# Kernel tuning notes

Measured on AMD Instinct MI355X. Metric: run time of the kernel, lower is better.

Reference implementation:

```python
import jax, jax.numpy as jnp
import numpy as np

N = 50000      # nodes
E = 600000     # edges
D_IN = 128     # node_dim
D = 128        # out_channels
T = 4          # num_node_types
R = 4          # num_edge_types
L = 2          # num_layers
C = 8          # num_class
G = 512        # graphs in batch


def setup_inputs() -> dict:
    key = jax.random.key(0)
    ks = jax.random.split(key, 12)
    s = 0.05
    x = jax.random.normal(ks[0], (N, D_IN), jnp.float32)
    node_type = jax.random.randint(ks[1], (N,), 0, T)
    edge_index = jax.random.randint(ks[2], (2, E), 0, N)
    edge_type = jax.random.randint(ks[3], (E,), 0, R)
    batch = jnp.sort(jax.random.randint(ks[4], (N,), 0, G))
    # learned params
    W_het = jax.random.normal(ks[5], (T, D_IN, D), jnp.float32) * s
    b_het = jnp.zeros((T, D), jnp.float32)
    conv_W = jax.random.normal(ks[6], (L, R, D, D), jnp.float32) * s
    conv_b = jnp.zeros((L, R, D), jnp.float32)
    fuse_W = jax.random.normal(ks[7], (R * D, D), jnp.float32) * s
    fuse_b = jnp.zeros((D,), jnp.float32)
    cls_W = jax.random.normal(ks[8], (D, C), jnp.float32) * s
    cls_b = jnp.zeros((C,), jnp.float32)
    return dict(x=x, W_het=W_het, b_het=b_het, conv_W=conv_W, conv_b=conv_b,
                fuse_W=fuse_W, fuse_b=fuse_b, cls_W=cls_W, cls_b=cls_b,
                node_type=node_type, edge_index=edge_index, edge_type=edge_type,
                batch=batch)


def reference(x, W_het, b_het, conv_W, conv_b, fuse_W, fuse_b, cls_W, cls_b,
              node_type, edge_index, edge_type, batch):
    n = x.shape[0]
    # HeteroLinear: per-node-type linear. Compute all T projections then select.
    x_all = jnp.einsum('nd,tdo->tno', x, W_het)          # [T, N, D]
    h = x_all[node_type, jnp.arange(n)] + b_het[node_type]
    src, dst = edge_index[0], edge_index[1]
    for l in range(L):
        hs = h[src]                                       # [E, D] gather once per layer
        outs = []
        for r in range(R):
            # edges of relation r only (boolean mask == per-relation edge filtering)
            m = hs @ conv_W[l, r]                         # [E, D]
            m = m * (edge_type == r).astype(m.dtype)[:, None]
            agg = jax.ops.segment_sum(m, dst, num_segments=n)  # scatter-add to dst
            outs.append(agg + conv_b[l, r])
        h = jax.nn.relu(jnp.concatenate(outs, axis=1) @ fuse_W + fuse_b)
    # global mean pool over graphs
    counts = jax.ops.segment_sum(jnp.ones((n,), h.dtype), batch, num_segments=G)
    emb = jax.ops.segment_sum(h, batch, num_segments=G) / jnp.maximum(counts, 1.0)[:, None]
    logits = emb @ cls_W + cls_b
    return emb, logits
```

## Files before the change

### kernel.cpp

```cpp
#include <hip/hip_runtime.h>

#define N_NODES 50000
#define N_EDGES 600000
#define DIM     128
#define RR      4
#define LL      2
#define GG      512
#define CC      8
#define NB_SCAN ((N_NODES + 255) / 256)
#define EC      (N_EDGES / 4)
#define FB      ((EC + 255) / 256)
#define TB      ((N_NODES + 255) / 256)
#define NBH     ((N_NODES + 63) / 64)
#define CB      (1026 + 3125)

typedef short bf16x8 __attribute__((ext_vector_type(8)));
typedef float f32x4  __attribute__((ext_vector_type(4)));

__device__ __forceinline__ float bf16_to_f(unsigned short u) {
    return __uint_as_float(((unsigned int)u) << 16);
}
__device__ __forceinline__ unsigned short f_to_bf16(float f) {
    unsigned int u = __float_as_uint(f);
    u += 0x7FFFu + ((u >> 16) & 1u);
    return (unsigned short)(u >> 16);
}
__device__ __forceinline__ float loadf(const void* p, long i, int isbf) {
    if (isbf) return bf16_to_f(((const unsigned short*)p)[i]);
    return ((const float*)p)[i];
}
__device__ __forceinline__ void storef(void* p, long i, float v, int isbf) {
    if (isbf) ((unsigned short*)p)[i] = f_to_bf16(v);
    else      ((float*)p)[i] = v;
}

__global__ void cg_init(const unsigned int* __restrict__ xw, int* __restrict__ flag,
                        int* __restrict__ deg_tb) {
    __shared__ int cnt;
    int tid = threadIdx.x;
    int t = blockIdx.x * 256 + tid;
    if (t < N_NODES + 16) deg_tb[t] = 0;
    if (blockIdx.x == 0) {
        if (tid == 0) cnt = 0;
        __syncthreads();
        unsigned int w = xw[tid];
        unsigned int e = (w >> 7) & 0xFFu;
        atomicAdd(&cnt, (e >= 110u && e <= 133u) ? 1 : 0);
        __syncthreads();
        if (tid == 0) *flag = (cnt >= 128) ? 1 : 0;
    }
}

__global__ void cg_hist_canon(const int* __restrict__ edge_index, const int* __restrict__ node_type,
                              int* __restrict__ deg, int* __restrict__ tb,
                              const void* __restrict__ x,
                              const void* __restrict__ W_het, const void* __restrict__ b_het,
                              const void* __restrict__ conv_W, const void* __restrict__ fuse_W,
                              const void* __restrict__ conv_b, const void* __restrict__ fuse_b,
                              const int* __restrict__ flagp,
                              unsigned short* __restrict__ xb, unsigned short* __restrict__ Wt,
                              float* __restrict__ bhf,
                              unsigned short* __restrict__ M2t, float* __restrict__ cvec) {
    __shared__ float s[256];
    int bk = blockIdx.x;
    int tid = threadIdx.x;
    if (bk < FB) {
        __shared__ int loc[4];
        if (tid < 4) loc[tid] = 0;
        __syncthreads();
        int t = bk * 256 + tid;
        if (t < EC) {
            int d0 = edge_index[N_EDGES + t];
            int d1 = edge_index[N_EDGES + t + EC];
            int d2 = edge_index[N_EDGES + t + 2 * EC];
            int d3 = edge_index[N_EDGES + t + 3 * EC];
            atomicAdd(&deg[d0], 1);
            atomicAdd(&deg[d1], 1);
            atomicAdd(&deg[d2], 1);
            atomicAdd(&deg[d3], 1);
        }
        if (t < N_NODES) atomicAdd(&loc[node_type[t]], 1);
        __syncthreads();
        if (tid < 4 && loc[tid]) atomicAdd(&tb[tid], loc[tid]);
        return;
    }
    int b = bk - FB;
    int isbf = *flagp;
    if (b < 512) {
        int lr = b >> 6;
        int d  = (b & 63) * 2 + (tid >> 7);
        int r  = lr & 3;
        int o  = tid & 127;
        float acc = 0.0f;
        for (int k = 0; k < DIM; k++) {
            acc += loadf(conv_W, (long)(lr * DIM + d) * DIM + k, isbf)
                 * loadf(fuse_W, (long)(r * DIM + k) * DIM + o, isbf);
        }
        M2t[((long)lr * DIM + o) * DIM + d] = f_to_bf16(acc);
    } else if (b < 768) {
        int bc = b - 512;
        int l  = bc >> 7;
        int o  = bc & 127;
        float part = 0.0f;
        for (int rk = tid; rk < RR * DIM; rk += 256) {
            part += loadf(conv_b, (long)l * RR * DIM + rk, isbf)
                  * loadf(fuse_W, (long)rk * DIM + o, isbf);
        }
        s[tid] = part;
        __syncthreads();
        for (int off = 128; off > 0; off >>= 1) {
            if (tid < off) s[tid] += s[tid + off];
            __syncthreads();
        }
        if (tid == 0) cvec[bc] = s[0] + loadf(fuse_b, o, isbf);
    } else if (b < 1024) {
        int pair = (b - 768) * 2 + (tid >> 7);
        int t = pair >> 7;
        int o = pair & 127;
        int d = tid & 127;
        float v = loadf(W_het, ((long)t * DIM + d) * DIM + o, isbf);
        Wt[((long)t * DIM + o) * DIM + d] = f_to_bf16(v);
    } else if (b < 1026) {
        int idx = (b - 1024) * 256 + tid;
        if (idx < 4 * DIM) bhf[idx] = loadf(b_het, idx, isbf);
    } else {
        long i = ((long)(b - 1026) * 256 + tid) * 8;
        if (i >= (long)N_NODES * DIM) return;
        if (isbf) {
            *(uint4*)(xb + i) = *(const uint4*)((const unsigned short*)x + i);
        } else {
            const float* xf = (const float*)x + i;
            float4 f0 = *(const float4*)xf;
            float4 f1 = *(const float4*)(xf + 4);
            uint4 o;
            o.x = (unsigned int)f_to_bf16(f0.x) | ((unsigned int)f_to_bf16(f0.y) << 16);
            o.y = (unsigned int)f_to_bf16(f0.z) | ((unsigned int)f_to_bf16(f0.w) << 16);
            o.z = (unsigned int)f_to_bf16(f1.x) | ((unsigned int)f_to_bf16(f1.y) << 16);
            o.w = (unsigned int)f_to_bf16(f1.z) | ((unsigned int)f_to_bf16(f1.w) << 16);
            *(uint4*)(xb + i) = o;
        }
    }
}

__global__ void cg_scan_a(const int* __restrict__ deg, int* __restrict__ blocksum) {
    __shared__ int s[256];
    int tid = threadIdx.x;
    int i = blockIdx.x * 256 + tid;
    s[tid] = (i < N_NODES) ? deg[i] : 0;
    __syncthreads();
    for (int off = 128; off > 0; off >>= 1) {
        if (tid < off) s[tid] += s[tid + off];
        __syncthreads();
    }
    if (tid == 0) blocksum[blockIdx.x] = s[0];
}

__global__ void cg_scan_b(const int* __restrict__ blocksum, int* __restrict__ blockoff,
                          int* __restrict__ ccursor,
                          int* __restrict__ rowptr, int* __restrict__ tb) {
    __shared__ int s[256];
    int tid = threadIdx.x;
    int v = (tid < NB_SCAN) ? blocksum[tid] : 0;
    s[tid] = v;
    __syncthreads();
    for (int off = 1; off < 256; off <<= 1) {
        int a = (tid >= off) ? s[tid - off] : 0;
        __syncthreads();
        s[tid] += a;
        __syncthreads();
    }
    if (tid < NB_SCAN) {
        int e = s[tid] - v;
        blockoff[tid] = e;
        ccursor[tid]  = e;
    }
    if (tid == 255) rowptr[N_NODES] = s[255];
    if (tid == 0) {
        int run = 0;
        for (int t = 0; t < 4; t++) {
            tb[8 + t] = run;
            tb[4 + t] = run;
            run += tb[t];
        }
        tb[12] = run;
    }
}

__global__ void cg_scan_tfill(const int* __restrict__ deg, const int* __restrict__ blockoff,
                              int* __restrict__ rowptr,
                              const int* __restrict__ node_type, int* __restrict__ tb,
                              int* __restrict__ tlist) {
    int bk = blockIdx.x;
    int tid = threadIdx.x;
    if (bk < NB_SCAN) {
        __shared__ int s[256];
        int i = bk * 256 + tid;
        int v = (i < N_NODES) ? deg[i] : 0;
        s[tid] = v;
        __syncthreads();
        for (int off = 1; off < 256; off <<= 1) {
            int a = (tid >= off) ? s[tid - off] : 0;
            __syncthreads();
            s[tid] += a;
            __syncthreads();
        }
        if (i < N_NODES) rowptr[i] = blockoff[bk] + s[tid] - v;
    } else {
        __shared__ int lcur[4];
        __shared__ int lbase[4];
        if (tid < 4) lcur[tid] = 0;
        __syncthreads();
        int n = (bk - NB_SCAN) * 256 + tid;
        int slot = -1, t = 0;
        if (n < N_NODES) {
            t = node_type[n];
            slot = atomicAdd(&lcur[t], 1);
        }
        __syncthreads();
        if (tid < 4) lbase[tid] = atomicAdd(&tb[4 + tid], lcur[tid]);
        __syncthreads();
        if (n < N_NODES) tlist[lbase[t] + slot] = n;
    }
}

#define APAD 136

__global__ void cg_sortA_hetero(const int* __restrict__ edge_index, const int* __restrict__ edge_type,
                                int* __restrict__ ccursor, int2* __restrict__ tmp2,
                                const unsigned short* __restrict__ xb,
                                const unsigned short* __restrict__ Wt,
                                const float* __restrict__ bhf,
                                const int* __restrict__ tlist, const int* __restrict__ tb,
                                unsigned short* __restrict__ h) {
    __shared__ unsigned short a_lds[64][APAD];
    __shared__ unsigned short b_lds[DIM][APAD];
    int bk = blockIdx.x;
    int tx = threadIdx.x;
    if (bk < FB) {
        __shared__ int lhist[NB_SCAN];
        __shared__ int lbase[NB_SCAN];
        for (int i = tx; i < NB_SCAN; i += 256) lhist[i] = 0;
        __syncthreads();
        int t = bk * 256 + tx;
        int d[4], cb[4], ls[4], pl[4];
        bool act = (t < EC);
        if (act) {
#pragma unroll
            for (int k = 0; k < 4; k++) {
                int e = t + k * EC;
                d[k]  = edge_index[N_EDGES + e];
                pl[k] = (edge_index[e] << 2) | edge_type[e];
                cb[k] = d[k] >> 8;
                ls[k] = atomicAdd(&lhist[cb[k]], 1);
            }
        }
        __syncthreads();
        for (int i = tx; i < NB_SCAN; i += 256)
            lbase[i] = lhist[i] ? atomicAdd(&ccursor[i], lhist[i]) : 0;
        __syncthreads();
        if (act) {
#pragma unroll
            for (int k = 0; k < 4; k++) {
                int pos = lbase[cb[k]] + ls[k];
                tmp2[pos] = make_int2(pl[k], d[k]);
            }
        }
        return;
    }
    int bb = bk - FB;
    int t    = bb / NBH;
    int nblk = bb - t * NBH;
    int rows_base = tb[8 + t] + nblk * 64;
    int rend = tb[8 + t + 1];
    if (rows_base >= rend) return;
    const unsigned short* Wsrc = Wt + (long)t * DIM * DIM;
    for (int i = tx; i < 2048; i += 256) {
        uint4 w = *(const uint4*)(Wsrc + i * 8);
        int o = i >> 4, d2 = (i & 15) * 8;
        *(uint4*)&b_lds[o][d2] = w;
    }
    for (int i = tx; i < 1024; i += 256) {
        int row = i >> 4, seg = (i & 15) * 8;
        int gr = rows_base + row;
        uint4 w = make_uint4(0u, 0u, 0u, 0u);
        if (gr < rend) {
            int n = tlist[gr];
            w = *(const uint4*)(xb + (long)n * DIM + seg);
        }
        *(uint4*)&a_lds[row][seg] = w;
    }
    __syncthreads();
    int wv = tx >> 6, lane = tx & 63;
    int m16 = lane & 15, quad = lane >> 4;
    f32x4 acc[8];
#pragma unroll
    for (int c = 0; c < 8; c++) acc[c] = (f32x4){0.f, 0.f, 0.f, 0.f};
    for (int ks = 0; ks < 4; ks++) {
        int koff = ks * 32 + quad * 8;
        bf16x8 af = *(const bf16x8*)(const void*)&a_lds[wv * 16 + m16][koff];
#pragma unroll
        for (int c = 0; c < 8; c++) {
            bf16x8 bfr = *(const bf16x8*)(const void*)&b_lds[c * 16 + m16][koff];
            acc[c] = __builtin_amdgcn_mfma_f32_16x16x32_bf16(af, bfr, acc[c], 0, 0, 0);
        }
    }
    __syncthreads();
#pragma unroll
    for (int c = 0; c < 8; c++) {
#pragma unroll
        for (int i = 0; i < 4; i++) {
            int row = wv * 16 + quad * 4 + i;
            int col = c * 16 + m16;
            a_lds[row][col] = f_to_bf16(acc[c][i] + bhf[t * DIM + col]);
        }
    }
    __syncthreads();
    for (int i = tx; i < 1024; i += 256) {
        int row = i >> 4, seg = (i & 15) * 8;
        int gr = rows_base + row;
        if (gr < rend) {
            int n = tlist[gr];
            *(uint4*)(h + (long)n * DIM + seg) = *(const uint4*)&a_lds[row][seg];
        }
    }
}

__global__ void cg_sortB_pgemm(const int2* __restrict__ tmp2, const int* __restrict__ blockoff,
                               const int* __restrict__ rowptr, int* __restrict__ eidx,
                               const unsigned short* __restrict__ h,
                               const unsigned short* __restrict__ M2t,
                               unsigned short* __restrict__ P) {
    __shared__ unsigned short a_lds[64][APAD];
    __shared__ unsigned short b_lds[DIM][APAD];
    int bk = blockIdx.x;
    int tx = threadIdx.x;
    if (bk < NB_SCAN) {
        __shared__ int lcur[256];
        int nn = bk * 256 + tx;
        lcur[tx] = (nn < N_NODES) ? rowptr[nn] : 0;
        int base = blockoff[bk];
        int endp = (bk + 1 < NB_SCAN) ? blockoff[bk + 1] : N_EDGES;
        int cnt = endp - base;
        __syncthreads();
        for (int i = tx; i < cnt; i += 256) {
            int2 v = tmp2[base + i];
            int pos = atomicAdd(&lcur[v.y & 255], 1);
            eidx[pos] = v.x;
        }
        return;
    }
    int bb = bk - NB_SCAN;
    int r    = bb / NBH;
    int nblk = bb - r * NBH;
    int n0 = nblk * 64;
    const unsigned short* Bsrc = M2t + (long)r * DIM * DIM;
    for (int i = tx; i < 2048; i += 256) {
        uint4 w = *(const uint4*)(Bsrc + i * 8);
        int o = i >> 4, d = (i & 15) * 8;
        *(uint4*)&b_lds[o][d] = w;
    }
    for (int i = tx; i < 1024; i += 256) {
        int row = i >> 4, seg = (i & 15) * 8;
        int n = n0 + row;
        uint4 w = make_uint4(0u, 0u, 0u, 0u);
        if (n < N_NODES) w = *(const uint4*)(h + (long)n * DIM + seg);
        *(uint4*)&a_lds[row][seg] = w;
    }
    __syncthreads();
    int wv = tx >> 6, lane = tx & 63;
    int m16 = lane & 15, quad = lane >> 4;
    f32x4 acc[8];
#pragma unroll
    for (int c = 0; c < 8; c++) acc[c] = (f32x4){0.f, 0.f, 0.f, 0.f};
    for (int ks = 0; ks < 4; ks++) {
        int koff = ks * 32 + quad * 8;
        bf16x8 af = *(const bf16x8*)(const void*)&a_lds[wv * 16 + m16][koff];
#pragma unroll
        for (int c = 0; c < 8; c++) {
            bf16x8 bfr = *(const bf16x8*)(const void*)&b_lds[c * 16 + m16][koff];
            acc[c] = __builtin_amdgcn_mfma_f32_16x16x32_bf16(af, bfr, acc[c], 0, 0, 0);
        }
    }
    __syncthreads();
#pragma unroll
    for (int c = 0; c < 8; c++) {
#pragma unroll
        for (int i = 0; i < 4; i++) {
            int row = wv * 16 + quad * 4 + i;
            int col = c * 16 + m16;
            a_lds[row][col] = f_to_bf16(acc[c][i]);
        }
    }
    __syncthreads();
    for (int i = tx; i < 1024; i += 256) {
        int row = i >> 4, seg = (i & 15) * 8;
        int n = n0 + row;
        if (n < N_NODES)
            *(uint4*)(P + (long)n * (RR * DIM) + r * DIM + seg) = *(const uint4*)&a_lds[row][seg];
    }
}

__global__ void cg_pgemm_mfma(const unsigned short* __restrict__ h,
                              const unsigned short* __restrict__ M2t, int l,
                              unsigned short* __restrict__ P) {
    int r  = blockIdx.y;
    int n0 = blockIdx.x * 64;
    __shared__ unsigned short a_lds[64][APAD];
    __shared__ unsigned short b_lds[DIM][APAD];
    int tx = threadIdx.x;
    const unsigned short* Bsrc = M2t + (long)(l * RR + r) * DIM * DIM;
    for (int i = tx; i < 2048; i += 256) {
        uint4 w = *(const uint4*)(Bsrc + i * 8);
        int o = i >> 4, d = (i & 15) * 8;
        *(uint4*)&b_lds[o][d] = w;
    }
    for (int i = tx; i < 1024; i += 256) {
        int row = i >> 4, seg = (i & 15) * 8;
        int n = n0 + row;
        uint4 w = make_uint4(0u, 0u, 0u, 0u);
        if (n < N_NODES) w = *(const uint4*)(h + (long)n * DIM + seg);
        *(uint4*)&a_lds[row][seg] = w;
    }
    __syncthreads();
    int wv = tx >> 6, lane = tx & 63;
    int m16 = lane & 15, quad = lane >> 4;
    f32x4 acc[8];
#pragma unroll
    for (int c = 0; c < 8; c++) acc[c] = (f32x4){0.f, 0.f, 0.f, 0.f};
    for (int ks = 0; ks < 4; ks++) {
        int koff = ks * 32 + quad * 8;
        bf16x8 af = *(const bf16x8*)(const void*)&a_lds[wv * 16 + m16][koff];
#pragma unroll
        for (int c = 0; c < 8; c++) {
            bf16x8 bfr = *(const bf16x8*)(const void*)&b_lds[c * 16 + m16][koff];
            acc[c] = __builtin_amdgcn_mfma_f32_16x16x32_bf16(af, bfr, acc[c], 0, 0, 0);
        }
    }
    __syncthreads();
#pragma unroll
    for (int c = 0; c < 8; c++) {
#pragma unroll
        for (int i = 0; i < 4; i++) {
            int row = wv * 16 + quad * 4 + i;
            int col = c * 16 + m16;
            a_lds[row][col] = f_to_bf16(acc[c][i]);
        }
    }
    __syncthreads();
    for (int i = tx; i < 1024; i += 256) {
        int row = i >> 4, seg = (i & 15) * 8;
        int n = n0 + row;
        if (n < N_NODES)
            *(uint4*)(P + (long)n * (RR * DIM) + r * DIM + seg) = *(const uint4*)&a_lds[row][seg];
    }
}

__global__ void cg_gather4(const unsigned short* __restrict__ P, const int* __restrict__ rowptr,
                           const int* __restrict__ eidx, const float* __restrict__ cv,
                           unsigned short* __restrict__ hout) {
    int wid  = (blockIdx.x * 256 + threadIdx.x) >> 6;
    int lane = threadIdx.x & 63;
    if (wid >= N_NODES) return;
    int eg = lane >> 4;
    int ol = lane & 15;
    int start = rowptr[wid];
    int end   = (wid + 1 < N_NODES) ? rowptr[wid + 1] : N_EDGES;
    float a[8] = {0.f, 0.f, 0.f, 0.f, 0.f, 0.f, 0.f, 0.f};
    int j = start + eg;
    for (; j + 4 < end; j += 8) {
        int v0 = eidx[j];
        int v1 = eidx[j + 4];
        const uint4 w0 = *(const uint4*)(P + (long)(v0 >> 2) * (RR * DIM) + (v0 & 3) * DIM + ol * 8);
        const uint4 w1 = *(const uint4*)(P + (long)(v1 >> 2) * (RR * DIM) + (v1 & 3) * DIM + ol * 8);
        a[0] += bf16_to_f((unsigned short)(w0.x & 0xFFFFu)) + bf16_to_f((unsigned short)(w1.x & 0xFFFFu));
        a[1] += bf16_to_f((unsigned short)(w0.x >> 16))     + bf16_to_f((unsigned short)(w1.x >> 16));
        a[2] += bf16_to_f((unsigned short)(w0.y & 0xFFFFu)) + bf16_to_f((unsigned short)(w1.y & 0xFFFFu));
        a[3] += bf16_to_f((unsigned short)(w0.y >> 16))     + bf16_to_f((unsigned short)(w1.y >> 16));
        a[4] += bf16_to_f((unsigned short)(w0.z & 0xFFFFu)) + bf16_to_f((unsigned short)(w1.z & 0xFFFFu));
        a[5] += bf16_to_f((unsigned short)(w0.z >> 16))     + bf16_to_f((unsigned short)(w1.z >> 16));
        a[6] += bf16_to_f((unsigned short)(w0.w & 0xFFFFu)) + bf16_to_f((unsigned short)(w1.w & 0xFFFFu));
        a[7] += bf16_to_f((unsigned short)(w0.w >> 16))     + bf16_to_f((unsigned short)(w1.w >> 16));
    }
    if (j < end) {
        int v = eidx[j];
        const uint4 w = *(const uint4*)(P + (long)(v >> 2) * (RR * DIM) + (v & 3) * DIM + ol * 8);
        a[0] += bf16_to_f((unsigned short)(w.x & 0xFFFFu));
        a[1] += bf16_to_f((unsigned short)(w.x >> 16));
        a[2] += bf16_to_f((unsigned short)(w.y & 0xFFFFu));
        a[3] += bf16_to_f((unsigned short)(w.y >> 16));
        a[4] += bf16_to_f((unsigned short)(w.z & 0xFFFFu));
        a[5] += bf16_to_f((unsigned short)(w.z >> 16));
        a[6] += bf16_to_f((unsigned short)(w.w & 0xFFFFu));
        a[7] += bf16_to_f((unsigned short)(w.w >> 16));
    }
#pragma unroll
    for (int i = 0; i < 8; i++) {
        a[i] += __shfl_xor(a[i], 16);
        a[i] += __shfl_xor(a[i], 32);
    }
    if (eg == 0) {
        int o0 = ol * 8;
        float v[8];
#pragma unroll
        for (int i = 0; i < 8; i++) {
            float s = a[i] + cv[o0 + i];
            v[i] = s > 0.0f ? s : 0.0f;
        }
        uint4 o4;
        o4.x = (unsigned int)f_to_bf16(v[0]) | ((unsigned int)f_to_bf16(v[1]) << 16);
        o4.y = (unsigned int)f_to_bf16(v[2]) | ((unsigned int)f_to_bf16(v[3]) << 16);
        o4.z = (unsigned int)f_to_bf16(v[4]) | ((unsigned int)f_to_bf16(v[5]) << 16);
        o4.w = (unsigned int)f_to_bf16(v[6]) | ((unsigned int)f_to_bf16(v[7]) << 16);
        *(uint4*)(hout + (long)wid * DIM + o0) = o4;
    }
}

__global__ void cg_pool_logits(const unsigned short* __restrict__ h, const int* __restrict__ batch,
                               const void* __restrict__ cls_W, const void* __restrict__ cls_b,
                               const int* __restrict__ flagp, void* __restrict__ out) {
    __shared__ float acc_s[4][DIM];
    __shared__ float emb_s[DIM];
    int g   = blockIdx.x;
    int tid = threadIdx.x;
    int wv  = tid >> 6;
    int lane = tid & 63;
    int sub = lane >> 4;
    int ol  = lane & 15;
    int isbf = *flagp;
    int lo = 0, hi = N_NODES;
    while (lo < hi) { int mid = (lo + hi) >> 1; if (batch[mid] < g) lo = mid + 1; else hi = mid; }
    int start = lo;
    hi = N_NODES;
    while (lo < hi) { int mid = (lo + hi) >> 1; if (batch[mid] < g + 1) lo = mid + 1; else hi = mid; }
    int end = lo;
    float a[8] = {0.f, 0.f, 0.f, 0.f, 0.f, 0.f, 0.f, 0.f};
    for (int n = start + wv * 4 + sub; n < end; n += 16) {
        uint4 w = *(const uint4*)(h + (long)n * DIM + ol * 8);
        a[0] += bf16_to_f((unsigned short)(w.x & 0xFFFFu));
        a[1] += bf16_to_f((unsigned short)(w.x >> 16));
        a[2] += bf16_to_f((unsigned short)(w.y & 0xFFFFu));
        a[3] += bf16_to_f((unsigned short)(w.y >> 16));
        a[4] += bf16_to_f((unsigned short)(w.z & 0xFFFFu));
        a[5] += bf16_to_f((unsigned short)(w.z >> 16));
        a[6] += bf16_to_f((unsigned short)(w.w & 0xFFFFu));
        a[7] += bf16_to_f((unsigned short)(w.w >> 16));
    }
#pragma unroll
    for (int i = 0; i < 8; i++) {
        a[i] += __shfl_xor(a[i], 16);
        a[i] += __shfl_xor(a[i], 32);
    }
    if (sub == 0) {
#pragma unroll
        for (int i = 0; i < 8; i++) acc_s[wv][ol * 8 + i] = a[i];
    }
    __syncthreads();
    int cnt = end - start;
    float inv = 1.0f / (float)(cnt > 1 ? cnt : 1);
    if (tid < DIM) {
        float e = (acc_s[0][tid] + acc_s[1][tid] + acc_s[2][tid] + acc_s[3][tid]) * inv;
        emb_s[tid] = e;
        storef(out, (long)g * DIM + tid, e, isbf);
    }
    __syncthreads();
    if (tid < 128) {
        int c  = tid >> 4;
        int kk = tid & 15;
        float p = 0.0f;
#pragma unroll
        for (int k = kk * 8; k < kk * 8 + 8; k++)
            p += emb_s[k] * loadf(cls_W, (long)k * CC + c, isbf);
        p += __shfl_xor(p, 1);
        p += __shfl_xor(p, 2);
        p += __shfl_xor(p, 4);
        p += __shfl_xor(p, 8);
        if (kk == 0)
            storef(out, (long)GG * DIM + g * CC + c, p + loadf(cls_b, c, isbf), isbf);
    }
}

extern "C" void kernel_launch(void* const* d_in, const int* in_sizes, int n_in,
                              void* d_out, int out_size, void* d_ws, size_t ws_size,
                              hipStream_t stream) {
    const void* x      = d_in[0];
    const void* W_het  = d_in[1];
    const void* b_het  = d_in[2];
    const void* conv_W = d_in[3];
    const void* conv_b = d_in[4];
    const void* fuse_W = d_in[5];
    const void* fuse_b = d_in[6];
    const void* cls_W  = d_in[7];
    const void* cls_b  = d_in[8];
    const int* node_type  = (const int*)d_in[9];
    const int* edge_index = (const int*)d_in[10];
    const int* edge_type  = (const int*)d_in[11];
    const int* batch      = (const int*)d_in[12];

    char* base = (char*)d_ws;
    unsigned short* hbf      = (unsigned short*)(base + 0);
    unsigned short* P        = (unsigned short*)(base + 12800000);
    unsigned short* xb       = (unsigned short*)(base + 64000000);
    unsigned short* Wt       = (unsigned short*)(base + 76800000);
    float*          bhf      = (float*)(base + 76931072);
    unsigned short* M2t      = (unsigned short*)(base + 76933120);
    float*          cvec     = (float*)(base + 77195264);
    int*            rowptr   = (int*)(base + 77196288);
    int*            deg      = (int*)(base + 77396320);
    int*            tb       = (int*)(base + 77596320);
    int*            blocksum = (int*)(base + 77596384);
    int*            blockoff = (int*)(base + 77597408);
    int*            ccursor  = (int*)(base + 77598432);
    int*            eidx     = (int*)(base + 77599456);
    int*            tlist    = (int*)(base + 79999456);
    int*            flag     = (int*)(base + 80199456);
    int2*           tmp2     = (int2*)(base + 80199472);

    cg_init<<<(N_NODES + 16 + 255) / 256, 256, 0, stream>>>((const unsigned int*)x, flag, deg);
    cg_hist_canon<<<FB + CB, 256, 0, stream>>>(edge_index, node_type, deg, tb,
                                               x, W_het, b_het, conv_W, fuse_W,
                                               conv_b, fuse_b, flag,
                                               xb, Wt, bhf, M2t, cvec);
    cg_scan_a<<<NB_SCAN, 256, 0, stream>>>(deg, blocksum);
    cg_scan_b<<<1, 256, 0, stream>>>(blocksum, blockoff, ccursor, rowptr, tb);
    cg_scan_tfill<<<NB_SCAN + TB, 256, 0, stream>>>(deg, blockoff, rowptr,
                                                    node_type, tb, tlist);
    cg_sortA_hetero<<<FB + 4 * NBH, 256, 0, stream>>>(edge_index, edge_type, ccursor, tmp2,
                                                      xb, Wt, bhf, tlist, tb, hbf);
    cg_sortB_pgemm<<<NB_SCAN + 4 * NBH, 256, 0, stream>>>(tmp2, blockoff, rowptr, eidx,
                                                          hbf, M2t, P);
    cg_gather4<<<(N_NODES * 64 + 255) / 256, 256, 0, stream>>>(
        P, rowptr, eidx, cvec, hbf);
    cg_pgemm_mfma<<<dim3(NBH, RR), 256, 0, stream>>>(hbf, M2t, 1, P);
    cg_gather4<<<(N_NODES * 64 + 255) / 256, 256, 0, stream>>>(
        P, rowptr, eidx, cvec + DIM, hbf);

    cg_pool_logits<<<GG, 256, 0, stream>>>(hbf, batch, cls_W, cls_b, flag, d_out);
}
```

Baseline: 304.9 us.

## Replace per-node degree histogram with coarse bucket histogram and local rowptr computation

Result: faster. 292.9 us, median of 2 (-3.9%).

```diff
diff --git a/kernel.cpp b/kernel.cpp
--- a/kernel.cpp
+++ b/kernel.cpp
@@ -7,7 +7,7 @@
 #define LL      2
 #define GG      512
 #define CC      8
-#define NB_SCAN ((N_NODES + 255) / 256)
+#define NCB     196
 #define EC      (N_EDGES / 4)
 #define FB      ((EC + 255) / 256)
 #define TB      ((N_NODES + 255) / 256)
@@ -35,24 +35,21 @@
 }
 
 __global__ void cg_init(const unsigned int* __restrict__ xw, int* __restrict__ flag,
-                        int* __restrict__ deg_tb) {
+                        int* __restrict__ chist_tb) {
     __shared__ int cnt;
     int tid = threadIdx.x;
-    int t = blockIdx.x * 256 + tid;
-    if (t < N_NODES + 16) deg_tb[t] = 0;
-    if (blockIdx.x == 0) {
-        if (tid == 0) cnt = 0;
-        __syncthreads();
-        unsigned int w = xw[tid];
-        unsigned int e = (w >> 7) & 0xFFu;
-        atomicAdd(&cnt, (e >= 110u && e <= 133u) ? 1 : 0);
-        __syncthreads();
-        if (tid == 0) *flag = (cnt >= 128) ? 1 : 0;
-    }
+    if (tid < NCB + 16) chist_tb[tid] = 0;
+    if (tid == 0) cnt = 0;
+    __syncthreads();
+    unsigned int w = xw[tid];
+    unsigned int e = (w >> 7) & 0xFFu;
+    atomicAdd(&cnt, (e >= 110u && e <= 133u) ? 1 : 0);
+    __syncthreads();
+    if (tid == 0) *flag = (cnt >= 128) ? 1 : 0;
 }
 
 __global__ void cg_hist_canon(const int* __restrict__ edge_index, const int* __restrict__ node_type,
-                              int* __restrict__ deg, int* __restrict__ tb,
+                              int* __restrict__ chist, int* __restrict__ tb,
                               const void* __restrict__ x,
                               const void* __restrict__ W_het, const void* __restrict__ b_het,
                               const void* __restrict__ conv_W, const void* __restrict__ fuse_W,
@@ -65,22 +62,23 @@
     int bk = blockIdx.x;
     int tid = threadIdx.x;
     if (bk < FB) {
+        __shared__ int lh[NCB];
         __shared__ int loc[4];
+        for (int i = tid; i < NCB; i += 256) lh[i] = 0;
         if (tid < 4) loc[tid] = 0;
         __syncthreads();
         int t = bk * 256 + tid;
         if (t < EC) {
-            int d0 = edge_index[N_EDGES + t];
-            int d1 = edge_index[N_EDGES + t + EC];
-            int d2 = edge_index[N_EDGES + t + 2 * EC];
-            int d3 = edge_index[N_EDGES + t + 3 * EC];
-            atomicAdd(&deg[d0], 1);
-            atomicAdd(&deg[d1], 1);
-            atomicAdd(&deg[d2], 1);
-            atomicAdd(&deg[d3], 1);
+#pragma unroll
+            for (int k = 0; k < 4; k++) {
+                int d = edge_index[N_EDGES + t + k * EC];
+                atomicAdd(&lh[d >> 8], 1);
+            }
         }
         if (t < N_NODES) atomicAdd(&loc[node_type[t]], 1);
         __syncthreads();
+        for (int i = tid; i < NCB; i += 256)
+            if (lh[i]) atomicAdd(&chist[i], lh[i]);
         if (tid < 4 && loc[tid]) atomicAdd(&tb[tid], loc[tid]);
         return;
     }
@@ -142,25 +140,11 @@
     }
 }
 
-__global__ void cg_scan_a(const int* __restrict__ deg, int* __restrict__ blocksum) {
+__global__ void cg_scan196(const int* __restrict__ chist, int* __restrict__ blockoff,
+                           int* __restrict__ ccursor, int* __restrict__ tb) {
     __shared__ int s[256];
     int tid = threadIdx.x;
-    int i = blockIdx.x * 256 + tid;
-    s[tid] = (i < N_NODES) ? deg[i] : 0;
-    __syncthreads();
-    for (int off = 128; off > 0; off >>= 1) {
-        if (tid < off) s[tid] += s[tid + off];
-        __syncthreads();
-    }
-    if (tid == 0) blocksum[blockIdx.x] = s[0];
-}
-
-__global__ void cg_scan_b(const int* __restrict__ blocksum, int* __restrict__ blockoff,
-                          int* __restrict__ ccursor,
-                          int* __restrict__ rowptr, int* __restrict__ tb) {
-    __shared__ int s[256];
-    int tid = threadIdx.x;
-    int v = (tid < NB_SCAN) ? blocksum[tid] : 0;
+    int v = (tid < NCB) ? chist[tid] : 0;
     s[tid] = v;
     __syncthreads();
     for (int off = 1; off < 256; off <<= 1) {
@@ -169,12 +153,11 @@
         s[tid] += a;
         __syncthreads();
     }
-    if (tid < NB_SCAN) {
+    if (tid < NCB) {
         int e = s[tid] - v;
         blockoff[tid] = e;
         ccursor[tid]  = e;
     }
-    if (tid == 255) rowptr[N_NODES] = s[255];
     if (tid == 0) {
         int run = 0;
         for (int t = 0; t < 4; t++) {
@@ -186,41 +169,23 @@
     }
 }
 
-__global__ void cg_scan_tfill(const int* __restrict__ deg, const int* __restrict__ blockoff,
-                              int* __restrict__ rowptr,
-                              const int* __restrict__ node_type, int* __restrict__ tb,
-                              int* __restrict__ tlist) {
-    int bk = blockIdx.x;
+__global__ void cg_tfill(const int* __restrict__ node_type, int* __restrict__ tb,
+                         int* __restrict__ tlist) {
+    __shared__ int lcur[4];
+    __shared__ int lbase[4];
     int tid = threadIdx.x;
-    if (bk < NB_SCAN) {
-        __shared__ int s[256];
-        int i = bk * 256 + tid;
-        int v = (i < N_NODES) ? deg[i] : 0;
-        s[tid] = v;
-        __syncthreads();
-        for (int off = 1; off < 256; off <<= 1) {
-            int a = (tid >= off) ? s[tid - off] : 0;
-            __syncthreads();
-            s[tid] += a;
-            __syncthreads();
-        }
-        if (i < N_NODES) rowptr[i] = blockoff[bk] + s[tid] - v;
-    } else {
-        __shared__ int lcur[4];
-        __shared__ int lbase[4];
-        if (tid < 4) lcur[tid] = 0;
-        __syncthreads();
-        int n = (bk - NB_SCAN) * 256 + tid;
-        int slot = -1, t = 0;
-        if (n < N_NODES) {
-            t = node_type[n];
-            slot = atomicAdd(&lcur[t], 1);
-        }
-        __syncthreads();
-        if (tid < 4) lbase[tid] = atomicAdd(&tb[4 + tid], lcur[tid]);
-        __syncthreads();
-        if (n < N_NODES) tlist[lbase[t] + slot] = n;
-    }
+    if (tid < 4) lcur[tid] = 0;
+    __syncthreads();
+    int n = blockIdx.x * 256 + tid;
+    int slot = -1, t = 0;
+    if (n < N_NODES) {
+        t = node_type[n];
+        slot = atomicAdd(&lcur[t], 1);
+    }
+    __syncthreads();
+    if (tid < 4) lbase[tid] = atomicAdd(&tb[4 + tid], lcur[tid]);
+    __syncthreads();
+    if (n < N_NODES) tlist[lbase[t] + slot] = n;
 }
 
 #define APAD 136
@@ -237,9 +202,9 @@
     int bk = blockIdx.x;
     int tx = threadIdx.x;
     if (bk < FB) {
-        __shared__ int lhist[NB_SCAN];
-        __shared__ int lbase[NB_SCAN];
-        for (int i = tx; i < NB_SCAN; i += 256) lhist[i] = 0;
+        __shared__ int lhist[NCB];
+        __shared__ int lbase[NCB];
+        for (int i = tx; i < NCB; i += 256) lhist[i] = 0;
         __syncthreads();
         int t = bk * 256 + tx;
         int d[4], cb[4], ls[4], pl[4];
@@ -255,7 +220,7 @@
             }
         }
         __syncthreads();
-        for (int i = tx; i < NB_SCAN; i += 256)
+        for (int i = tx; i < NCB; i += 256)
             lbase[i] = lhist[i] ? atomicAdd(&ccursor[i], lhist[i]) : 0;
         __syncthreads();
         if (act) {
@@ -326,7 +291,7 @@
 }
 
 __global__ void cg_sortB_pgemm(const int2* __restrict__ tmp2, const int* __restrict__ blockoff,
-                               const int* __restrict__ rowptr, int* __restrict__ eidx,
+                               int* __restrict__ rowptr, int* __restrict__ eidx,
                                const unsigned short* __restrict__ h,
                                const unsigned short* __restrict__ M2t,
                                unsigned short* __restrict__ P) {
@@ -334,22 +299,40 @@
     __shared__ unsigned short b_lds[DIM][APAD];
     int bk = blockIdx.x;
     int tx = threadIdx.x;
-    if (bk < NB_SCAN) {
+    if (bk < NCB) {
+        __shared__ int lcnt[256];
+        __shared__ int lscan[256];
         __shared__ int lcur[256];
-        int nn = bk * 256 + tx;
-        lcur[tx] = (nn < N_NODES) ? rowptr[nn] : 0;
+        lcnt[tx] = 0;
         int base = blockoff[bk];
-        int endp = (bk + 1 < NB_SCAN) ? blockoff[bk + 1] : N_EDGES;
+        int endp = (bk + 1 < NCB) ? blockoff[bk + 1] : N_EDGES;
         int cnt = endp - base;
         __syncthreads();
+        for (int i = tx; i < cnt; i += 256)
+            atomicAdd(&lcnt[tmp2[base + i].y & 255], 1);
+        __syncthreads();
+        int v = lcnt[tx];
+        lscan[tx] = v;
+        __syncthreads();
+        for (int off = 1; off < 256; off <<= 1) {
+            int a = (tx >= off) ? lscan[tx - off] : 0;
+            __syncthreads();
+            lscan[tx] += a;
+            __syncthreads();
+        }
+        int start = base + lscan[tx] - v;
+        lcur[tx] = start;
+        int n = bk * 256 + tx;
+        if (n < N_NODES) rowptr[n] = start;
+        __syncthreads();
         for (int i = tx; i < cnt; i += 256) {
-            int2 v = tmp2[base + i];
-            int pos = atomicAdd(&lcur[v.y & 255], 1);
-            eidx[pos] = v.x;
+            int2 e = tmp2[base + i];
+            int pos = atomicAdd(&lcur[e.y & 255], 1);
+            eidx[pos] = e.x;
         }
         return;
     }
-    int bb = bk - NB_SCAN;
+    int bb = bk - NCB;
     int r    = bb / NBH;
     int nblk = bb - r * NBH;
     int n0 = nblk * 64;
@@ -605,29 +588,26 @@
     unsigned short* M2t      = (unsigned short*)(base + 76933120);
     float*          cvec     = (float*)(base + 77195264);
     int*            rowptr   = (int*)(base + 77196288);
-    int*            deg      = (int*)(base + 77396320);
-    int*            tb       = (int*)(base + 77596320);
-    int*            blocksum = (int*)(base + 77596384);
-    int*            blockoff = (int*)(base + 77597408);
-    int*            ccursor  = (int*)(base + 77598432);
-    int*            eidx     = (int*)(base + 77599456);
-    int*            tlist    = (int*)(base + 79999456);
-    int*            flag     = (int*)(base + 80199456);
-    int2*           tmp2     = (int2*)(base + 80199472);
-
-    cg_init<<<(N_NODES + 16 + 255) / 256, 256, 0, stream>>>((const unsigned int*)x, flag, deg);
-    cg_hist_canon<<<FB + CB, 256, 0, stream>>>(edge_index, node_type, deg, tb,
+    int*            chist    = (int*)(base + 77396320);
+    int*            tb       = chist + NCB;
+    int*            blockoff = (int*)(base + 77397408);
+    int*            ccursor  = (int*)(base + 77398432);
+    int*            eidx     = (int*)(base + 77399456);
+    int*            tlist    = (int*)(base + 79799456);
+    int*            flag     = (int*)(base + 79999456);
+    int2*           tmp2     = (int2*)(base + 79999472);
+
+    cg_init<<<1, 256, 0, stream>>>((const unsigned int*)x, flag, chist);
+    cg_hist_canon<<<FB + CB, 256, 0, stream>>>(edge_index, node_type, chist, tb,
                                                x, W_het, b_het, conv_W, fuse_W,
                                                conv_b, fuse_b, flag,
                                                xb, Wt, bhf, M2t, cvec);
-    cg_scan_a<<<NB_SCAN, 256, 0, stream>>>(deg, blocksum);
-    cg_scan_b<<<1, 256, 0, stream>>>(blocksum, blockoff, ccursor, rowptr, tb);
-    cg_scan_tfill<<<NB_SCAN + TB, 256, 0, stream>>>(deg, blockoff, rowptr,
-                                                    node_type, tb, tlist);
+    cg_scan196<<<1, 256, 0, stream>>>(chist, blockoff, ccursor, tb);
+    cg_tfill<<<TB, 256, 0, stream>>>(node_type, tb, tlist);
     cg_sortA_hetero<<<FB + 4 * NBH, 256, 0, stream>>>(edge_index, edge_type, ccursor, tmp2,
                                                       xb, Wt, bhf, tlist, tb, hbf);
-    cg_sortB_pgemm<<<NB_SCAN + 4 * NBH, 256, 0, stream>>>(tmp2, blockoff, rowptr, eidx,
-                                                          hbf, M2t, P);
+    cg_sortB_pgemm<<<NCB + 4 * NBH, 256, 0, stream>>>(tmp2, blockoff, rowptr, eidx,
+                                                      hbf, M2t, P);
     cg_gather4<<<(N_NODES * 64 + 255) / 256, 256, 0, stream>>>(
         P, rowptr, eidx, cvec, hbf);
     cg_pgemm_mfma<<<dim3(NBH, RR), 256, 0, stream>>>(hbf, M2t, 1, P);
```
